# Optimization experiments

Measured on AMD Instinct MI355X. Metric: run time of the kernel, lower is better.

The kernel has to match this reference:

```python
import jax, jax.numpy as jnp
import numpy as np

B, C, N = 4, 32, 256
D_IN, D_EMB, K = 512, 1024, 4096  # input_dim, llm_embedding_dim, codebook_size
EPS = 1e-12


def setup_inputs() -> dict:
    key = jax.random.key(0)
    ks = jax.random.split(key, 6)
    s_in = float(1.0 / np.sqrt(D_IN))
    s_emb = float(1.0 / np.sqrt(D_EMB))
    return {
        "x": jax.random.normal(ks[0], (B, C, N, D_IN), jnp.float32),
        # nn.Linear(input_dim, llm_embedding_dim): weight [out, in], uniform(-1/sqrt(in), 1/sqrt(in))
        "w_in": jax.random.uniform(ks[1], (D_EMB, D_IN), jnp.float32, -s_in, s_in),
        "b_in": jax.random.uniform(ks[2], (D_EMB,), jnp.float32, -s_in, s_in),
        "w_out": jax.random.uniform(ks[3], (D_IN, D_EMB), jnp.float32, -s_emb, s_emb),
        "b_out": jax.random.uniform(ks[4], (D_IN,), jnp.float32, -s_emb, s_emb),
        # frozen LLM-embedding codebook (copied from llm_embedding_bank, requires_grad=False)
        "codebook": jax.random.normal(ks[5], (K, D_EMB), jnp.float32),
    }


def _rotate_to(src, tgt):
    # Rotation trick (arXiv:2410.06424, sec 4.2) as in vector-quantize-pytorch.
    # Forward value equals tgt; gradient flows through src via a (detached)
    # Householder rotation + scaling.
    n_src = jnp.linalg.norm(src, axis=-1, keepdims=True)
    n_tgt = jnp.linalg.norm(tgt, axis=-1, keepdims=True)
    u = jax.lax.stop_gradient(src / jnp.maximum(n_src, EPS))   # unit src, detached
    q = tgt / jnp.maximum(n_tgt, EPS)                          # unit tgt (codebook: no grad)
    w = u + q
    w = jax.lax.stop_gradient(w / jnp.maximum(jnp.linalg.norm(w, axis=-1, keepdims=True), EPS))
    rot = (src
           - 2.0 * jnp.sum(src * w, -1, keepdims=True) * w
           + 2.0 * jnp.sum(src * u, -1, keepdims=True) * q)
    return rot * jax.lax.stop_gradient(n_tgt / jnp.maximum(n_src, EPS))


def reference(x, w_in, b_in, w_out, b_out, codebook):
    Bb, Cc, Nn, _ = x.shape
    # input projection, flatten channels x patches into token axis
    z = jnp.einsum('bcnd,ed->bcne', x, w_in) + b_in          # [B, C, N, D_EMB]
    z = z.reshape(Bb, Cc * Nn, -1)                           # [B, T, D_EMB]
    # squared euclidean distances to codebook: ||z||^2 - 2 z.c + ||c||^2
    dists = (jnp.sum(z * z, -1, keepdims=True)
             - 2.0 * jnp.einsum('bte,ke->btk', z, codebook)
             + jnp.sum(codebook * codebook, -1))             # [B, T, K]
    indices = jnp.argmin(dists, axis=-1)                     # [B, T] int
    q = codebook[indices]                                    # gather [B, T, D_EMB]
    quantized = _rotate_to(z, q)                             # == q in value
    # commitment loss (commitment_weight = 1.0); codebook frozen -> only commit term
    aux_loss = jnp.mean((jax.lax.stop_gradient(quantized) - z) ** 2)
    out = jnp.einsum('bte,de->btd', quantized, w_out) + b_out
    return (out.reshape(Bb, Cc, Nn, -1),
            indices,
            quantized.reshape(Bb, Cc, Nn, -1),
            aux_loss)
```

## Files before the change

kernel.cpp:

```cpp
#include <hip/hip_runtime.h>

#define M_TOK 32768
#define DIN   512
#define DEMB  1024
#define KC    4096

#define IDX_OFF ((size_t)M_TOK * DIN)
#define Q_OFF   (IDX_OFF + M_TOK)
#define AUX_OFF (Q_OFF + (size_t)M_TOK * DEMB)

typedef _Float16 f16x8 __attribute__((ext_vector_type(8)));
typedef _Float16 f16x4 __attribute__((ext_vector_type(4)));
typedef float f32x4 __attribute__((ext_vector_type(4)));

__device__ inline void gload16(const void* g, void* s) {
    __builtin_amdgcn_global_load_lds((const __attribute__((address_space(1))) void*)g,
                                     (__attribute__((address_space(3))) void*)s, 16, 0, 0);
}

__device__ inline unsigned umin2(unsigned a, unsigned b) { return a < b ? a : b; }
__device__ inline unsigned umax2(unsigned a, unsigned b) { return a > b ? a : b; }

__device__ inline float block_reduce_sum_256(float v) {
#pragma unroll
    for (int off = 32; off > 0; off >>= 1) v += __shfl_down(v, off);
    __shared__ float smem[4];
    const int lane = threadIdx.x & 63;
    const int w = threadIdx.x >> 6;
    if (lane == 0) smem[w] = v;
    __syncthreads();
    return smem[0] + smem[1] + smem[2] + smem[3];
}

__global__ __launch_bounds__(256) void prep_all(const float* __restrict__ cb,
                                                const float* __restrict__ w_out,
                                                const float* __restrict__ w_in,
                                                _Float16* __restrict__ cbf,
                                                _Float16* __restrict__ wok,
                                                _Float16* __restrict__ wpk,
                                                _Float16* __restrict__ cbp,
                                                float* __restrict__ cn2p,
                                                float* __restrict__ aux) {
    const int b = blockIdx.x;
    if (b < 4096) {
        if (b == 0 && threadIdx.x == 0) *aux = 0.0f;
        const float4 v = reinterpret_cast<const float4*>(cb + (size_t)b * DEMB)[threadIdx.x];
        f16x4 h;
        h[0] = (_Float16)v.x; h[1] = (_Float16)v.y; h[2] = (_Float16)v.z; h[3] = (_Float16)v.w;
        reinterpret_cast<f16x4*>(cbf + (size_t)b * DEMB)[threadIdx.x] = h;
        float s = v.x * v.x + v.y * v.y + v.z * v.z + v.w * v.w;
        s = block_reduce_sum_256(s);
        if (threadIdx.x == 0) cn2p[b] = 0.5f * s + 1024.0f;
    } else if (b < 4352) {
        const int id = (b - 4096) * 256 + threadIdx.x;
        const int l = id & 63;
        const int c16 = (id >> 6) & 31;
        const int kk = id >> 11;
        const int col = c16 * 16 + (l & 15);
        const int kb = kk * 32 + (l >> 4) * 8;
        const float* src = w_out + (size_t)col * DEMB + kb;
        const float4 a = *reinterpret_cast<const float4*>(src);
        const float4 b4 = *reinterpret_cast<const float4*>(src + 4);
        f16x8 h;
        h[0] = (_Float16)a.x; h[1] = (_Float16)a.y; h[2] = (_Float16)a.z; h[3] = (_Float16)a.w;
        h[4] = (_Float16)b4.x; h[5] = (_Float16)b4.y; h[6] = (_Float16)b4.z; h[7] = (_Float16)b4.w;
        *reinterpret_cast<f16x8*>(wok + (size_t)id * 8) = h;
    } else if (b < 6400) {
        const int id = (b - 4352) * 256 + threadIdx.x;
        const int c16 = id >> 11;
        const int rem = id & 2047;
        const int kk = rem >> 6;
        const int l = rem & 63;
        const int lgq = l >> 4, lcq = l & 15;
        const float* src = cb + ((size_t)(c16 * 16 + lcq)) * DEMB + kk * 32 + lgq * 8;
        const float4 a = *reinterpret_cast<const float4*>(src);
        const float4 b4 = *reinterpret_cast<const float4*>(src + 4);
        f16x8 h;
        h[0] = (_Float16)a.x; h[1] = (_Float16)a.y; h[2] = (_Float16)a.z; h[3] = (_Float16)a.w;
        h[4] = (_Float16)b4.x; h[5] = (_Float16)b4.y; h[6] = (_Float16)b4.z; h[7] = (_Float16)b4.w;
        const int ntile = c16 >> 2, nn = c16 & 3;
        const size_t off = ((size_t)(kk * 256 + ntile * 4 + nn)) * 64 + l;
        *reinterpret_cast<f16x8*>(cbp + off * 8) = h;
    } else {
        const int id = (b - 6400) * 256 + threadIdx.x;
        const int l = id & 63;
        const int hl = (id >> 6) & 1;
        const int c16 = (id >> 7) & 63;
        const int kk = id >> 13;
        const int col = c16 * 16 + (l & 15);
        const int kb = kk * 32 + (l >> 4) * 8;
        const float* src = w_in + (size_t)col * DIN + kb;
        const float4 a = *reinterpret_cast<const float4*>(src);
        const float4 b4 = *reinterpret_cast<const float4*>(src + 4);
        const float e[8] = {a.x, a.y, a.z, a.w, b4.x, b4.y, b4.z, b4.w};
        f16x8 o;
#pragma unroll
        for (int j = 0; j < 8; ++j) {
            const _Float16 hv = (_Float16)e[j];
            o[j] = hl ? (_Float16)((e[j] - (float)hv) * 2048.0f) : hv;
        }
        *reinterpret_cast<f16x8*>(wpk + (size_t)id * 8) = o;
    }
}

__global__ void __launch_bounds__(512)
__attribute__((amdgpu_waves_per_eu(2, 2)))
zgemm_stream(const float* __restrict__ x,
             const _Float16* __restrict__ wpk,
             const float* __restrict__ bin,
             float* __restrict__ zq,
             _Float16* __restrict__ zf) {
    extern __shared__ _Float16 sm[];
    _Float16* Ah = sm;
    _Float16* Al = sm + 32768;
    const int t = threadIdx.x;
    const int w = t >> 6, l = t & 63;
    const int lg = l >> 4, lc = l & 15;
    const int m0 = blockIdx.x * 64;

    {
        const int r = t >> 3;
        const int c0 = t & 7;
#pragma unroll
        for (int i = 0; i < 8; ++i) {
            const int c = c0 + i * 8;
            const float* px = x + (size_t)(m0 + r) * DIN + c * 8;
            const float4 a = *reinterpret_cast<const float4*>(px);
            const float4 b4 = *reinterpret_cast<const float4*>(px + 4);
            const float e[8] = {a.x, a.y, a.z, a.w, b4.x, b4.y, b4.z, b4.w};
            f16x8 h, lo;
#pragma unroll
            for (int j = 0; j < 8; ++j) {
                const _Float16 hv = (_Float16)e[j];
                h[j] = hv;
                lo[j] = (_Float16)((e[j] - (float)hv) * 2048.0f);
            }
            const int swz = (c & 0x30) | ((c ^ r) & 15);
            *reinterpret_cast<f16x8*>(Ah + (size_t)(r * 64 + swz) * 8) = h;
            *reinterpret_cast<f16x8*>(Al + (size_t)(r * 64 + swz) * 8) = lo;
        }
    }

    const char* ztb = (const char*)sm;
    int lbase[4][4];
#pragma unroll
    for (int m = 0; m < 4; ++m)
#pragma unroll
        for (int j = 0; j < 4; ++j)
            lbase[m][j] = (m * 16 + lc) * 1024 + ((((j * 4) | lg) ^ lc) & 15) * 16;

    const char* pL = (const char*)wpk + w * 4096 + l * 16;

    f16x8 bh[2][2], bl[2][2];
#pragma unroll
    for (int s = 0; s < 2; ++s)
#pragma unroll
        for (int n = 0; n < 2; ++n) {
            bh[s][n] = *reinterpret_cast<const f16x8*>(pL + s * 131072 + n * 2048);
            bl[s][n] = *reinterpret_cast<const f16x8*>(pL + s * 131072 + n * 2048 + 1024);
        }

    __syncthreads();

    f16x8 ah[2][4], al[2][4];
#pragma unroll
    for (int m = 0; m < 4; ++m) {
        ah[0][m] = *reinterpret_cast<const f16x8*>(ztb + lbase[m][0]);
        al[0][m] = *reinterpret_cast<const f16x8*>(ztb + 65536 + lbase[m][0]);
    }

    unsigned boff = 2u * 131072u;
    for (int p = 0; p < 4; ++p) {
        f32x4 acc1[4][2], acc2[4][2];
#pragma unroll
        for (int n = 0; n < 2; ++n) {
            const float bb = bin[p * 256 + w * 32 + n * 16 + lc];
#pragma unroll
            for (int m = 0; m < 4; ++m) {
                acc1[m][n] = (f32x4){bb, bb, bb, bb};
                acc2[m][n] = (f32x4){0.f, 0.f, 0.f, 0.f};
            }
        }
        const unsigned wrapAdd = (unsigned)((p < 3 ? 1 : -3) * 32768 - 15 * 131072);
#pragma unroll
        for (int kk = 0; kk < 16; ++kk) {
            const int nk = (kk + 1) & 15;
#pragma unroll
            for (int m = 0; m < 4; ++m) {
                ah[(kk + 1) & 1][m] = *reinterpret_cast<const f16x8*>(
                    ztb + lbase[m][nk & 3] + ((nk >> 2) << 8));
                al[(kk + 1) & 1][m] = *reinterpret_cast<const f16x8*>(
                    ztb + 65536 + lbase[m][nk & 3] + ((nk >> 2) << 8));
            }
            __builtin_amdgcn_s_setprio(1);
#pragma unroll
            for (int m = 0; m < 4; ++m)
#pragma unroll
                for (int n = 0; n < 2; ++n) {
                    acc1[m][n] = __builtin_amdgcn_mfma_f32_16x16x32_f16(
                        ah[kk & 1][m], bh[kk & 1][n], acc1[m][n], 0, 0, 0);
                    acc2[m][n] = __builtin_amdgcn_mfma_f32_16x16x32_f16(
                        ah[kk & 1][m], bl[kk & 1][n], acc2[m][n], 0, 0, 0);
                    acc2[m][n] = __builtin_amdgcn_mfma_f32_16x16x32_f16(
                        al[kk & 1][m], bh[kk & 1][n], acc2[m][n], 0, 0, 0);
                }
            __builtin_amdgcn_s_setprio(0);
#pragma unroll
            for (int n = 0; n < 2; ++n) {
                bh[kk & 1][n] = *reinterpret_cast<const f16x8*>(pL + boff + n * 2048);
                bl[kk & 1][n] = *reinterpret_cast<const f16x8*>(pL + boff + n * 2048 + 1024);
            }
            boff += (kk == 13) ? wrapAdd : 131072u;
        }
#pragma unroll
        for (int n = 0; n < 2; ++n) {
            const int col = p * 256 + w * 32 + n * 16 + lc;
#pragma unroll
            for (int m = 0; m < 4; ++m)
#pragma unroll
                for (int rg = 0; rg < 4; ++rg) {
                    const int row = m0 + m * 16 + lg * 4 + rg;
                    const float z = acc1[m][n][rg] + acc2[m][n][rg] * (1.0f / 2048.0f);
                    zq[(size_t)row * DEMB + col] = z;
                    zf[(size_t)row * DEMB + col] = (_Float16)(-z);
                }
        }
    }
}

__global__ void __launch_bounds__(512)
__attribute__((amdgpu_waves_per_eu(2, 2)))
dist_refine(const _Float16* __restrict__ zf,
            const _Float16* __restrict__ cbp,
            const float* __restrict__ cn2p,
            const float* __restrict__ cb,
            float* __restrict__ zq,
            float* __restrict__ idx_f,
            int* __restrict__ idx_i,
            float* __restrict__ aux) {
    extern __shared__ _Float16 zt[];
    const int t = threadIdx.x;
    const int w = t >> 6, l = t & 63;
    const int lg = l >> 4, lc = l & 15;
    const int m0 = blockIdx.x * 64;

    {
        const int r0 = t >> 7;
        const int ch = t & 127;
#pragma unroll
        for (int i = 0; i < 16; ++i) {
            const int row = i * 4 + r0;
            const int sch = (ch & 0x70) | ((ch ^ row) & 15);
            gload16(zf + (((size_t)(m0 + row)) << 10) + sch * 8,
                    zt + ((size_t)(i * 512 + t)) * 8);
        }
    }

    const char* ztb = (const char*)zt;
    int lbase[4][4];
#pragma unroll
    for (int m = 0; m < 4; ++m)
#pragma unroll
        for (int j = 0; j < 4; ++j)
            lbase[m][j] = (m * 16 + lc) * 2048 + ((((j * 4) | lg) ^ lc) << 4);

    unsigned k0[16], k1[16];
#pragma unroll
    for (int r = 0; r < 16; ++r) { k0[r] = 0xFFFFFFFFu; k1[r] = 0xFFFFFFFFu; }

    const char* pL = (const char*)cbp + l * 16;

    f16x8 bf[4][4];
    {
#pragma unroll
        for (int s = 0; s < 4; ++s)
#pragma unroll
            for (int n = 0; n < 4; ++n)
                bf[s][n] = *reinterpret_cast<const f16x8*>(pL + s * 262144 + w * 4096 + n * 1024);
    }
    __syncthreads();

    f16x8 af[4][4];
#pragma unroll
    for (int s = 0; s < 2; ++s)
#pragma unroll
        for (int m = 0; m < 4; ++m)
            af[s][m] = *reinterpret_cast<const f16x8*>(ztb + lbase[m][s] + ((s & 28) << 6));

    unsigned boff = (unsigned)(w * 4096 + 4 * 262144);
    for (int nt8 = 0; nt8 < 8; ++nt8) {
        const int ntile = nt8 * 8 + w;
        const unsigned wrapAdd = (unsigned)((nt8 < 7 ? 8 : -56) * 4096 - 31 * 262144);
        const int colb = ntile * 64;
        unsigned colw[4];
        float c2[4];
#pragma unroll
        for (int n = 0; n < 4; ++n) {
            colw[n] = (unsigned)(colb + n * 16 + lc);
            c2[n] = cn2p[colw[n]];
        }
        f32x4 acc[4][4];
#pragma unroll
        for (int m = 0; m < 4; ++m)
#pragma unroll
            for (int n = 0; n < 4; ++n)
                acc[m][n] = (f32x4){c2[n], c2[n], c2[n], c2[n]};

#pragma unroll
        for (int kk = 0; kk < 32; ++kk) {
            const int nk2 = (kk + 2) & 31;
#pragma unroll
            for (int m = 0; m < 4; ++m)
                af[(kk + 2) & 3][m] = *reinterpret_cast<const f16x8*>(
                    ztb + lbase[m][nk2 & 3] + ((nk2 & 28) << 6));
            __builtin_amdgcn_s_setprio(1);
#pragma unroll
            for (int m = 0; m < 4; ++m)
#pragma unroll
                for (int n = 0; n < 4; ++n)
                    acc[m][n] = __builtin_amdgcn_mfma_f32_16x16x32_f16(
                        af[kk & 3][m], bf[kk & 3][n], acc[m][n], 0, 0, 0);
            __builtin_amdgcn_s_setprio(0);
#pragma unroll
            for (int n = 0; n < 4; ++n)
                bf[kk & 3][n] = *reinterpret_cast<const f16x8*>(pL + boff + n * 1024);
            boff += (kk == 27) ? wrapAdd : 262144u;
        }

#pragma unroll
        for (int n = 0; n < 4; ++n) {
#pragma unroll
            for (int m = 0; m < 4; ++m)
#pragma unroll
                for (int rg = 0; rg < 4; ++rg) {
                    const unsigned key =
                        (__float_as_uint(acc[m][n][rg]) & 0xFFFFF000u) | colw[n];
                    const int r = m * 4 + rg;
                    const unsigned kmax = umax2(k0[r], key);
                    k0[r] = umin2(k0[r], key);
                    k1[r] = umin2(k1[r], kmax);
                }
        }
    }
#pragma unroll
    for (int off = 1; off < 16; off <<= 1) {
#pragma unroll
        for (int r = 0; r < 16; ++r) {
            const unsigned b0 = __shfl_xor(k0[r], off);
            const unsigned b1 = __shfl_xor(k1[r], off);
            const unsigned lo = umin2(k0[r], b0);
            const unsigned hi = umax2(k0[r], b0);
            k0[r] = lo;
            k1[r] = umin2(hi, umin2(k1[r], b1));
        }
    }

    __syncthreads();
    unsigned* pks = (unsigned*)zt;
    if (lc == 0) {
#pragma unroll
        for (int m = 0; m < 4; ++m)
#pragma unroll
            for (int rg = 0; rg < 4; ++rg) {
                const int r = m * 4 + rg;
                const int tloc = m * 16 + lg * 4 + rg;
                pks[(w * 2 + 0) * 64 + tloc] = k0[r];
                pks[(w * 2 + 1) * 64 + tloc] = k1[r];
            }
    }
    __syncthreads();

    float asum = 0.0f;
    for (int i = 0; i < 8; ++i) {
        const int tloc = w * 8 + i;
        const int tok = m0 + tloc;
        float4* zp = reinterpret_cast<float4*>(zq + ((size_t)tok << 10));
        float4 zr[4];
#pragma unroll
        for (int j = 0; j < 4; ++j) zr[j] = zp[l + j * 64];

        float zn = 0.0f;
#pragma unroll
        for (int j = 0; j < 4; ++j) {
            zn = fmaf(zr[j].x, zr[j].x, zn);
            zn = fmaf(zr[j].y, zr[j].y, zn);
            zn = fmaf(zr[j].z, zr[j].z, zn);
            zn = fmaf(zr[j].w, zr[j].w, zn);
        }
#pragma unroll
        for (int off = 1; off < 64; off <<= 1) zn += __shfl_xor(zn, off);

        unsigned v = 0xFFFFFFFFu;
        if (l < 16) v = pks[l * 64 + tloc];

        float bestd = 3.4e38f;
        int besti = 0x7fffffff;
#pragma unroll
        for (int s = 0; s < 4; ++s) {
            unsigned mv = v;
#pragma unroll
            for (int off = 1; off < 64; off <<= 1) mv = umin2(mv, __shfl_xor(mv, off));
            if (v == mv) v = 0xFFFFFFFFu;
            const int mi = (int)(mv & 0xFFFu);
            const float4* cp = reinterpret_cast<const float4*>(cb + ((size_t)mi << 10));
            float s4 = 0.0f;
#pragma unroll
            for (int j = 0; j < 4; ++j) {
                const float4 c = cp[l + j * 64];
                s4 = fmaf(zr[j].x, c.x, s4);
                s4 = fmaf(zr[j].y, c.y, s4);
                s4 = fmaf(zr[j].z, c.z, s4);
                s4 = fmaf(zr[j].w, c.w, s4);
            }
#pragma unroll
            for (int off = 1; off < 64; off <<= 1) s4 += __shfl_xor(s4, off);
            const float d = cn2p[mi] - s4;
            if (d < bestd || (d == bestd && mi < besti)) { bestd = d; besti = mi; }
        }
        const float4* cpb = reinterpret_cast<const float4*>(cb + ((size_t)besti << 10));
#pragma unroll
        for (int j = 0; j < 4; ++j) zp[l + j * 64] = cpb[l + j * 64];

        if (l == 0) {
            idx_f[tok] = (float)besti;
            idx_i[tok] = besti;
            asum += 2.0f * bestd - 2048.0f + zn;
        }
    }
    if (l == 0) atomicAdd(aux, asum * (1.0f / 33554432.0f));
}

__global__ void __launch_bounds__(512)
__attribute__((amdgpu_waves_per_eu(2, 2)))
outgemm_stream(const _Float16* __restrict__ cbf,
               const _Float16* __restrict__ wok,
               const float* __restrict__ bout,
               const int* __restrict__ idx,
               float* __restrict__ out) {
    extern __shared__ _Float16 at[];
    const int t = threadIdx.x;
    const int w = t >> 6, l = t & 63;
    const int lg = l >> 4, lc = l & 15;
    const int m0 = blockIdx.x * 64;

    {
        const int r0 = t >> 7;
        const int ch = t & 127;
#pragma unroll
        for (int i = 0; i < 16; ++i) {
            const int row = i * 4 + r0;
            const int gi = idx[m0 + row];
            const int sch = (ch & 0x70) | ((ch ^ row) & 15);
            gload16(cbf + (((size_t)gi) << 10) + sch * 8,
                    at + ((size_t)(i * 512 + t)) * 8);
        }
    }

    const char* ztb = (const char*)at;
    int lbase[4][4];
#pragma unroll
    for (int m = 0; m < 4; ++m)
#pragma unroll
        for (int j = 0; j < 4; ++j)
            lbase[m][j] = (m * 16 + lc) * 2048 + ((((j * 4) | lg) ^ lc) << 4);

    const char* pL = (const char*)wok + l * 16;

    f16x8 bf[4][4];
    {
#pragma unroll
        for (int s = 0; s < 4; ++s)
#pragma unroll
            for (int n = 0; n < 4; ++n)
                bf[s][n] = *reinterpret_cast<const f16x8*>(pL + s * 32768 + w * 4096 + n * 1024);
    }
    __syncthreads();

    f16x8 af[4][4];
#pragma unroll
    for (int s = 0; s < 2; ++s)
#pragma unroll
        for (int m = 0; m < 4; ++m)
            af[s][m] = *reinterpret_cast<const f16x8*>(ztb + lbase[m][s] + ((s & 28) << 6));

    f32x4 acc[4][4];
#pragma unroll
    for (int n = 0; n < 4; ++n) {
        const float bb = bout[w * 64 + n * 16 + lc];
#pragma unroll
        for (int m = 0; m < 4; ++m)
            acc[m][n] = (f32x4){bb, bb, bb, bb};
    }

    unsigned boff = (unsigned)(w * 4096 + 4 * 32768);
#pragma unroll
    for (int kk = 0; kk < 32; ++kk) {
        const int nk2 = (kk + 2) & 31;
#pragma unroll
        for (int m = 0; m < 4; ++m)
            af[(kk + 2) & 3][m] = *reinterpret_cast<const f16x8*>(
                ztb + lbase[m][nk2 & 3] + ((nk2 & 28) << 6));
        __builtin_amdgcn_s_setprio(1);
#pragma unroll
        for (int m = 0; m < 4; ++m)
#pragma unroll
            for (int n = 0; n < 4; ++n)
                acc[m][n] = __builtin_amdgcn_mfma_f32_16x16x32_f16(
                    af[kk & 3][m], bf[kk & 3][n], acc[m][n], 0, 0, 0);
        __builtin_amdgcn_s_setprio(0);
#pragma unroll
        for (int n = 0; n < 4; ++n)
            bf[kk & 3][n] = *reinterpret_cast<const f16x8*>(pL + boff + n * 1024);
        boff += (kk == 27) ? (unsigned)(-(28 * 32768)) : 32768u;
    }

#pragma unroll
    for (int n = 0; n < 4; ++n) {
        const int col = w * 64 + n * 16 + lc;
#pragma unroll
        for (int m = 0; m < 4; ++m)
#pragma unroll
            for (int rg = 0; rg < 4; ++rg) {
                const int row = m0 + m * 16 + lg * 4 + rg;
                out[(size_t)row * DIN + col] = acc[m][n][rg];
            }
    }
}

extern "C" void kernel_launch(void* const* d_in, const int* in_sizes, int n_in,
                              void* d_out, int out_size, void* d_ws, size_t ws_size,
                              hipStream_t stream) {
    const float* x = (const float*)d_in[0];
    const float* w_in = (const float*)d_in[1];
    const float* b_in = (const float*)d_in[2];
    const float* w_out = (const float*)d_in[3];
    const float* b_out = (const float*)d_in[4];
    const float* cb = (const float*)d_in[5];

    float* out = (float*)d_out;
    float* idx_f = out + IDX_OFF;
    float* zq = out + Q_OFF;
    float* aux = out + AUX_OFF;
    _Float16* zf = (_Float16*)d_out;

    char* ws = (char*)d_ws;
    float* cn2p = (float*)ws;
    int* idx_i = (int*)(ws + 16384);
    _Float16* cbf = (_Float16*)(ws + 4341760);
    _Float16* cbp = (_Float16*)(ws + 12730368);
    _Float16* wpk = (_Float16*)(ws + 21118976);
    _Float16* wok = (_Float16*)(ws + 23216128);

    prep_all<<<6912, 256, 0, stream>>>(cb, w_out, w_in, cbf, wok, wpk, cbp, cn2p, aux);
    zgemm_stream<<<M_TOK / 64, 512, 131072, stream>>>(x, wpk, b_in, zq, zf);
    dist_refine<<<M_TOK / 64, 512, 131072, stream>>>(zf, cbp, cn2p, cb, zq, idx_f, idx_i, aux);
    outgemm_stream<<<M_TOK / 64, 512, 131072, stream>>>(cbf, wok, b_out, idx_i, out);
}
```

Measured before the change: 493.8 us.

## Fuse output GEMM into distance/refine kernel using LDS-held indices

Merges the output-projection GEMM into the distance/argmin refinement kernel. Each block keeps its 64 selected codebook indices in shared memory and reuses the same LDS buffer to gather the fp16 codeword rows, then runs the MFMA output GEMM. This removes one kernel launch and the global round-trip of the index array, and lets the tail of one phase overlap with other blocks. The cost is a longer fused kernel with higher register pressure, which could hurt occupancy or scheduling.

```diff
diff --git a/kernel.cpp b/kernel.cpp
--- a/kernel.cpp
+++ b/kernel.cpp
@@ -230,15 +230,19 @@
 
 __global__ void __launch_bounds__(512)
 __attribute__((amdgpu_waves_per_eu(2, 2)))
-dist_refine(const _Float16* __restrict__ zf,
-            const _Float16* __restrict__ cbp,
-            const float* __restrict__ cn2p,
-            const float* __restrict__ cb,
-            float* __restrict__ zq,
-            float* __restrict__ idx_f,
-            int* __restrict__ idx_i,
-            float* __restrict__ aux) {
+dist_refine_out(const _Float16* __restrict__ zf,
+                const _Float16* __restrict__ cbp,
+                const float* __restrict__ cn2p,
+                const float* __restrict__ cb,
+                const _Float16* __restrict__ cbf,
+                const _Float16* __restrict__ wok,
+                const float* __restrict__ bout,
+                float* __restrict__ zq,
+                float* __restrict__ idx_f,
+                float* __restrict__ out,
+                float* __restrict__ aux) {
     extern __shared__ _Float16 zt[];
+    __shared__ int idxs[64];
     const int t = threadIdx.x;
     const int w = t >> 6, l = t & 63;
     const int lg = l >> 4, lc = l & 15;
@@ -423,95 +427,70 @@
 
         if (l == 0) {
             idx_f[tok] = (float)besti;
-            idx_i[tok] = besti;
+            idxs[tloc] = besti;
             asum += 2.0f * bestd - 2048.0f + zn;
         }
     }
     if (l == 0) atomicAdd(aux, asum * (1.0f / 33554432.0f));
-}
-
-__global__ void __launch_bounds__(512)
-__attribute__((amdgpu_waves_per_eu(2, 2)))
-outgemm_stream(const _Float16* __restrict__ cbf,
-               const _Float16* __restrict__ wok,
-               const float* __restrict__ bout,
-               const int* __restrict__ idx,
-               float* __restrict__ out) {
-    extern __shared__ _Float16 at[];
-    const int t = threadIdx.x;
-    const int w = t >> 6, l = t & 63;
-    const int lg = l >> 4, lc = l & 15;
-    const int m0 = blockIdx.x * 64;
-
+
+    __syncthreads();
     {
         const int r0 = t >> 7;
         const int ch = t & 127;
 #pragma unroll
         for (int i = 0; i < 16; ++i) {
             const int row = i * 4 + r0;
-            const int gi = idx[m0 + row];
+            const int gi = idxs[row];
             const int sch = (ch & 0x70) | ((ch ^ row) & 15);
             gload16(cbf + (((size_t)gi) << 10) + sch * 8,
-                    at + ((size_t)(i * 512 + t)) * 8);
-        }
-    }
-
-    const char* ztb = (const char*)at;
-    int lbase[4][4];
-#pragma unroll
-    for (int m = 0; m < 4; ++m)
-#pragma unroll
-        for (int j = 0; j < 4; ++j)
-            lbase[m][j] = (m * 16 + lc) * 2048 + ((((j * 4) | lg) ^ lc) << 4);
-
-    const char* pL = (const char*)wok + l * 16;
-
-    f16x8 bf[4][4];
-    {
-#pragma unroll
-        for (int s = 0; s < 4; ++s)
-#pragma unroll
-            for (int n = 0; n < 4; ++n)
-                bf[s][n] = *reinterpret_cast<const f16x8*>(pL + s * 32768 + w * 4096 + n * 1024);
-    }
-    __syncthreads();
-
-    f16x8 af[4][4];
+                    zt + ((size_t)(i * 512 + t)) * 8);
+        }
+    }
+    const char* pLo = (const char*)wok + l * 16;
+    f16x8 bfo[4][4];
+#pragma unroll
+    for (int s = 0; s < 4; ++s)
+#pragma unroll
+        for (int n = 0; n < 4; ++n)
+            bfo[s][n] = *reinterpret_cast<const f16x8*>(pLo + s * 32768 + w * 4096 + n * 1024);
+    __syncthreads();
+
+    f16x8 afo[4][4];
 #pragma unroll
     for (int s = 0; s < 2; ++s)
 #pragma unroll
         for (int m = 0; m < 4; ++m)
-            af[s][m] = *reinterpret_cast<const f16x8*>(ztb + lbase[m][s] + ((s & 28) << 6));
-
-    f32x4 acc[4][4];
+            afo[s][m] = *reinterpret_cast<const f16x8*>(ztb + lbase[m][s] + ((s & 28) << 6));
+
+    f32x4 acco[4][4];
 #pragma unroll
     for (int n = 0; n < 4; ++n) {
         const float bb = bout[w * 64 + n * 16 + lc];
 #pragma unroll
         for (int m = 0; m < 4; ++m)
-            acc[m][n] = (f32x4){bb, bb, bb, bb};
-    }
-
-    unsigned boff = (unsigned)(w * 4096 + 4 * 32768);
+            acco[m][n] = (f32x4){bb, bb, bb, bb};
+    }
+
+    unsigned bo = (unsigned)(w * 4096 + 4 * 32768);
 #pragma unroll
     for (int kk = 0; kk < 32; ++kk) {
         const int nk2 = (kk + 2) & 31;
 #pragma unroll
         for (int m = 0; m < 4; ++m)
-            af[(kk + 2) & 3][m] = *reinterpret_cast<const f16x8*>(
+            afo[(kk + 2) & 3][m] = *reinterpret_cast<const f16x8*>(
                 ztb + lbase[m][nk2 & 3] + ((nk2 & 28) << 6));
         __builtin_amdgcn_s_setprio(1);
 #pragma unroll
         for (int m = 0; m < 4; ++m)
 #pragma unroll
             for (int n = 0; n < 4; ++n)
-                acc[m][n] = __builtin_amdgcn_mfma_f32_16x16x32_f16(
-                    af[kk & 3][m], bf[kk & 3][n], acc[m][n], 0, 0, 0);
+                acco[m][n] = __builtin_amdgcn_mfma_f32_16x16x32_f16(
+                    afo[kk & 3][m], bfo[kk & 3][n], acco[m][n], 0, 0, 0);
         __builtin_amdgcn_s_setprio(0);
 #pragma unroll
         for (int n = 0; n < 4; ++n)
-            bf[kk & 3][n] = *reinterpret_cast<const f16x8*>(pL + boff + n * 1024);
-        boff += (kk == 27) ? (unsigned)(-(28 * 32768)) : 32768u;
+            bfo[kk & 3][n] = *reinterpret_cast<const f16x8*>(pLo + bo + n * 1024);
+        bo += (kk == 27) ? (unsigned)(-(28 * 32768)) : 32768u;
     }
 
 #pragma unroll
@@ -522,7 +501,7 @@
 #pragma unroll
             for (int rg = 0; rg < 4; ++rg) {
                 const int row = m0 + m * 16 + lg * 4 + rg;
-                out[(size_t)row * DIN + col] = acc[m][n][rg];
+                out[(size_t)row * DIN + col] = acco[m][n][rg];
             }
     }
 }
@@ -545,7 +524,6 @@
 
     char* ws = (char*)d_ws;
     float* cn2p = (float*)ws;
-    int* idx_i = (int*)(ws + 16384);
     _Float16* cbf = (_Float16*)(ws + 4341760);
     _Float16* cbp = (_Float16*)(ws + 12730368);
     _Float16* wpk = (_Float16*)(ws + 21118976);
@@ -553,6 +531,6 @@
 
     prep_all<<<6912, 256, 0, stream>>>(cb, w_out, w_in, cbf, wok, wpk, cbp, cn2p, aux);
     zgemm_stream<<<M_TOK / 64, 512, 131072, stream>>>(x, wpk, b_in, zq, zf);
-    dist_refine<<<M_TOK / 64, 512, 131072, stream>>>(zf, cbp, cn2p, cb, zq, idx_f, idx_i, aux);
-    outgemm_stream<<<M_TOK / 64, 512, 131072, stream>>>(cbf, wok, b_out, idx_i, out);
+    dist_refine_out<<<M_TOK / 64, 512, 131072, stream>>>(
+        zf, cbp, cn2p, cb, cbf, wok, b_out, zq, idx_f, out, aux);
 }
```

Measured after the change: 488.0 us (median of 2 runs). About the same (-1.2%).
